# Kernel optimization log

Hardware: AMD Instinct MI355X
Metric: run time of the kernel (lower is better)

## Reference

```python
import jax, jax.numpy as jnp
import numpy as np


def setup_inputs() -> dict:
    key = jax.random.key(0)
    k1, k2, k3, k4, k5 = jax.random.split(key, 5)
    B, S, E, H, D = 8, 1024, 1024, 8, 128  # batch, seq, embed, heads, hidden/head
    stdv = 1.0 / np.sqrt(D)
    return {
        "k": jax.random.normal(k1, (B, S, E), jnp.float32),
        "q": jax.random.normal(k2, (B, S, E), jnp.float32),
        "flag": 0,  # False: project q through w_qx
        "w_kx": jax.random.uniform(k3, (H, E, D), jnp.float32, -stdv, stdv),
        "w_qx": jax.random.uniform(k4, (H, E, D), jnp.float32, -stdv, stdv),
        "proj_w": jax.random.normal(k5, (E, H * D), jnp.float32) * 0.02,  # out_dim = embed_dim
        "proj_b": jnp.zeros((E,), jnp.float32),
    }


def reference(k, q, flag, w_kx, w_qx, proj_w, proj_b):
    H, E, D = w_kx.shape
    B, Sk, _ = k.shape
    Sq = q.shape[1]
    # per-head tanh projections: [H, B, S, D]
    kx = jnp.tanh(jnp.einsum("bse,hed->hbsd", k, w_kx))
    if flag:
        qx = jnp.broadcast_to(q[None], (H,) + q.shape)  # q already in hidden space
    else:
        qx = jnp.tanh(jnp.einsum("bse,hed->hbsd", q, w_qx))
    # scaled dot product scores [H, B, Sq, Sk]
    score = jnp.einsum("hbqd,hbkd->hbqk", qx, kx) / jnp.sqrt(jnp.float32(D))
    attn = jax.nn.softmax(score, axis=-1)
    out = jnp.einsum("hbqk,hbkd->hbqd", attn, kx)  # [H, B, Sq, D]
    # concat heads: [B, Sq, H*D], then output projection (dropout p=0 is identity)
    out = jnp.transpose(out, (1, 2, 0, 3)).reshape(B, Sq, H * D)
    return out @ proj_w.T + proj_b
```

## Files before the change

### kernel.cpp

```cpp
#include <hip/hip_runtime.h>

typedef unsigned short u16;
typedef unsigned int u32;
typedef __bf16 bf16x8 __attribute__((ext_vector_type(8)));
typedef float f32x4 __attribute__((ext_vector_type(4)));

#define MFMA16(a, b, c) __builtin_amdgcn_mfma_f32_16x16x32_bf16(a, b, c, 0, 0, 0)
#define EXP2(x) __builtin_amdgcn_exp2f(x)

typedef const void __attribute__((address_space(1)))* gas1_t;
typedef void __attribute__((address_space(3)))* las3_t;

__device__ __forceinline__ void gload16(const void* g, void* l) {
  __builtin_amdgcn_global_load_lds((gas1_t)g, (las3_t)l, 16, 0, 0);
}

__device__ __forceinline__ u16 f2bf(float f) {
  union { float f; u32 u; } v; v.f = f;
  u32 r = v.u + 0x7FFFu + ((v.u >> 16) & 1u);
  return (u16)(r >> 16);
}

__device__ __forceinline__ float fast_tanh(float x) {
  float xc = fminf(fmaxf(x, -20.f), 20.f);
  float t = EXP2(xc * 2.885390081777927f);
  return (t - 1.0f) * __builtin_amdgcn_rcpf(t + 1.0f);
}

__global__ __launch_bounds__(256) void cvt_kernel(const float* __restrict__ in,
                                                  u16* __restrict__ out, int n8) {
  int i = blockIdx.x * blockDim.x + threadIdx.x;
  int stride = gridDim.x * blockDim.x;
  for (; i < n8; i += stride) {
    const float4* p = (const float4*)(in + (size_t)i * 8);
    float4 a = p[0], b = p[1];
    u16 t[8];
    t[0] = f2bf(a.x); t[1] = f2bf(a.y); t[2] = f2bf(a.z); t[3] = f2bf(a.w);
    t[4] = f2bf(b.x); t[5] = f2bf(b.y); t[6] = f2bf(b.z); t[7] = f2bf(b.w);
    *(uint4*)(out + (size_t)i * 8) = *(uint4*)t;
  }
}

__global__ __launch_bounds__(256) void wtrans_kernel(const float* __restrict__ w,
                                                     u16* __restrict__ wT) {
  __shared__ float t[64][65];
  int h = blockIdx.z;
  int e0 = blockIdx.x * 64, d0 = blockIdx.y * 64;
  const float* src = w + (size_t)h * 1024 * 128;
  u16* dst = wT + (size_t)h * 128 * 1024;
  int tid = threadIdx.x;
  {
    int row = tid >> 2, c0 = (tid & 3) * 16;
#pragma unroll
    for (int i = 0; i < 4; ++i) {
      float4 v = *(const float4*)(src + (size_t)(e0 + row) * 128 + d0 + c0 + i * 4);
      t[row][c0 + i * 4 + 0] = v.x;
      t[row][c0 + i * 4 + 1] = v.y;
      t[row][c0 + i * 4 + 2] = v.z;
      t[row][c0 + i * 4 + 3] = v.w;
    }
  }
  __syncthreads();
  {
    int dl = tid >> 2, c0 = (tid & 3) * 16;
    u16 tmp[16];
#pragma unroll
    for (int i = 0; i < 16; ++i) tmp[i] = f2bf(t[c0 + i][dl]);
    u16* o = dst + (size_t)(d0 + dl) * 1024 + e0 + c0;
    *(uint4*)o = *(uint4*)tmp;
    *(uint4*)(o + 8) = *(uint4*)(tmp + 8);
  }
}

__device__ __forceinline__ void gemm_core128(const u16* Abase, const u16* Bbase,
                                             int K, u16* Alds, u16* Blds,
                                             f32x4 (&acc)[4][4]) {
  const int tid = threadIdx.x, lane = tid & 63, wid = tid >> 6;
  const int wr = wid >> 1, wc = wid & 1;
  const int nkt = K >> 6;
  for (int kt = 0; kt < nkt; ++kt) {
#pragma unroll
    for (int i = 0; i < 4; ++i) {
      int cIdx = (wid * 4 + i) * 64 + lane;
      int row = cIdx >> 3, slot = cIdx & 7;
      int src = slot ^ (row & 7);
      gload16((const char*)Abase + ((size_t)row * K + kt * 64 + src * 8) * 2,
              (char*)Alds + (wid * 4 + i) * 1024);
      gload16((const char*)Bbase + ((size_t)row * K + kt * 64 + src * 8) * 2,
              (char*)Blds + (wid * 4 + i) * 1024);
    }
    __syncthreads();
#pragma unroll
    for (int kc = 0; kc < 2; ++kc) {
      bf16x8 af[4], bb[4];
#pragma unroll
      for (int f = 0; f < 4; ++f) {
        int arow = wr * 64 + f * 16 + (lane & 15);
        int ch = kc * 4 + (lane >> 4);
        af[f] = *(const bf16x8*)(Alds + arow * 64 + ((ch ^ (arow & 7)) << 3));
        int brow = wc * 64 + f * 16 + (lane & 15);
        bb[f] = *(const bf16x8*)(Blds + brow * 64 + ((ch ^ (brow & 7)) << 3));
      }
#pragma unroll
      for (int mf = 0; mf < 4; ++mf)
#pragma unroll
        for (int nf = 0; nf < 4; ++nf)
          acc[mf][nf] = MFMA16(af[mf], bb[nf], acc[mf][nf]);
    }
    __syncthreads();
  }
}

__global__ __launch_bounds__(256) void gemm_tanh_kernel(
    const u16* __restrict__ Ak, const u16* __restrict__ Aq,
    const u16* __restrict__ wTk, const u16* __restrict__ wTq,
    u16* __restrict__ kxo, u16* __restrict__ qxo) {
  __shared__ alignas(16) u16 Alds[128 * 64];
  __shared__ alignas(16) u16 Blds[128 * 64];
  const u16* A; const u16* W; u16* C;
  if (blockIdx.z == 0) { A = Ak; W = wTk; C = kxo; }
  else { A = Aq; W = wTq; C = qxo; }
  int h = blockIdx.y;
  int mBase = blockIdx.x * 128;
  f32x4 acc[4][4];
#pragma unroll
  for (int i = 0; i < 4; ++i)
#pragma unroll
    for (int j = 0; j < 4; ++j) acc[i][j] = (f32x4){0.f, 0.f, 0.f, 0.f};
  gemm_core128(A + (size_t)mBase * 1024, W + (size_t)h * 128 * 1024, 1024,
               Alds, Blds, acc);
  const int lane = threadIdx.x & 63, wid = threadIdx.x >> 6;
  const int wr = wid >> 1, wc = wid & 1;
  u16* Ch = C + (size_t)h * 8192 * 128;
#pragma unroll
  for (int mf = 0; mf < 4; ++mf)
#pragma unroll
    for (int nf = 0; nf < 4; ++nf)
#pragma unroll
      for (int j = 0; j < 4; ++j) {
        int m = mBase + wr * 64 + mf * 16 + ((lane >> 4) << 2) + j;
        int d = wc * 64 + nf * 16 + (lane & 15);
        Ch[(size_t)m * 128 + d] = f2bf(fast_tanh(acc[mf][nf][j]));
      }
}

__global__ __launch_bounds__(256) void transpose_kernel(const u16* __restrict__ kx,
                                                        u16* __restrict__ kxT) {
  __shared__ u16 t[64][72];
  int hb = blockIdx.z;
  const u16* src = kx + (size_t)hb * 1024 * 128;
  u16* dst = kxT + (size_t)hb * 128 * 1024;
  int s0 = blockIdx.x * 64, d0 = blockIdx.y * 64;
  int tid = threadIdx.x;
#pragma unroll
  for (int r = 0; r < 2; ++r) {
    int row = r * 32 + (tid >> 3), c8 = (tid & 7) * 8;
    uint4 v = *(const uint4*)(src + (size_t)(s0 + row) * 128 + d0 + c8);
    *(uint4*)&t[row][c8] = v;
  }
  __syncthreads();
#pragma unroll
  for (int r = 0; r < 2; ++r) {
    int dl = r * 32 + (tid >> 3), s8 = (tid & 7) * 8;
    u16 tmp[8];
#pragma unroll
    for (int i = 0; i < 8; ++i) tmp[i] = t[s8 + i][dl];
    *(uint4*)(dst + (size_t)(d0 + dl) * 1024 + s0 + s8) = *(uint4*)tmp;
  }
}

__global__ __launch_bounds__(256, 2) void attn_kernel(const u16* __restrict__ qx,
                                                      const u16* __restrict__ kx,
                                                      const u16* __restrict__ kxT,
                                                      u16* __restrict__ X) {
  __shared__ alignas(16) u16 Klds[2][64 * 128];
  __shared__ alignas(16) u16 Vlds[2][128 * 64];
  __shared__ alignas(16) u16 Plds[4][32 * 64];
  const int tid = threadIdx.x, lane = tid & 63, wid = tid >> 6;
  const int hb = blockIdx.x, qt = blockIdx.y, h = hb >> 3, b = hb & 7;
  const u16* qxh = qx + ((size_t)h * 8192 + (size_t)b * 1024) * 128;
  const u16* kxh = kx + ((size_t)h * 8192 + (size_t)b * 1024) * 128;
  const u16* kxTh = kxT + (size_t)hb * 128 * 1024;
  const int q0 = qt * 128 + wid * 32;
  const float SC = 0.08838834764831845f * 1.44269504088896340f;

#define STAGE(buf, kt_)                                                        \
  do {                                                                         \
    _Pragma("unroll") for (int i_ = 0; i_ < 4; ++i_) {                         \
      int cIdx = (wid * 4 + i_) * 64 + lane;                                   \
      {                                                                        \
        int row = cIdx >> 4, slot = cIdx & 15;                                 \
        int src = slot ^ (row & 7);                                            \
        gload16((const char*)kxh + (size_t)((kt_) * 64 + row) * 256 + src * 16,\
                (char*)&Klds[buf][0] + (wid * 4 + i_) * 1024);                 \
      }                                                                        \
      {                                                                        \
        int row = cIdx >> 3, slot = cIdx & 7;                                  \
        int src = slot ^ (row & 7);                                            \
        gload16((const char*)kxTh + (size_t)row * 2048 + (kt_) * 128 + src * 16,\
                (char*)&Vlds[buf][0] + (wid * 4 + i_) * 1024);                 \
      }                                                                        \
    }                                                                          \
  } while (0)

  bf16x8 qa[2][4];
#pragma unroll
  for (int mf = 0; mf < 2; ++mf)
#pragma unroll
    for (int kc = 0; kc < 4; ++kc)
      qa[mf][kc] = *(const bf16x8*)(qxh + (size_t)(q0 + mf * 16 + (lane & 15)) * 128
                                    + kc * 32 + (lane >> 4) * 8);

  f32x4 os[2][8];
#pragma unroll
  for (int i = 0; i < 2; ++i)
#pragma unroll
    for (int j = 0; j < 8; ++j) os[i][j] = (f32x4){0.f, 0.f, 0.f, 0.f};
  float lsum[8];
#pragma unroll
  for (int i = 0; i < 8; ++i) lsum[i] = 0.f;

  u16* Pw = &Plds[wid][0];

  STAGE(0, 0);

  for (int kt = 0; kt < 16; ++kt) {
    const int cur = kt & 1;
    if (kt < 15) {
      STAGE(cur ^ 1, kt + 1);
      asm volatile("s_waitcnt vmcnt(8)" ::: "memory");
    } else {
      asm volatile("s_waitcnt vmcnt(0)" ::: "memory");
    }
    __builtin_amdgcn_s_barrier();

    const u16* Kc = &Klds[cur][0];
    const u16* Vc = &Vlds[cur][0];

    f32x4 sa[2][4];
#pragma unroll
    for (int i = 0; i < 2; ++i)
#pragma unroll
      for (int j = 0; j < 4; ++j) sa[i][j] = (f32x4){0.f, 0.f, 0.f, 0.f};
#pragma unroll
    for (int kc = 0; kc < 4; ++kc) {
      bf16x8 kb[4];
#pragma unroll
      for (int nf = 0; nf < 4; ++nf) {
        int row = nf * 16 + (lane & 15);
        int ch = kc * 4 + (lane >> 4);
        kb[nf] = *(const bf16x8*)(Kc + row * 128 + ((ch ^ (row & 7)) << 3));
      }
#pragma unroll
      for (int mf = 0; mf < 2; ++mf)
#pragma unroll
        for (int nf = 0; nf < 4; ++nf)
          sa[mf][nf] = MFMA16(qa[mf][kc], kb[nf], sa[mf][nf]);
    }

#pragma unroll
    for (int mf = 0; mf < 2; ++mf)
#pragma unroll
      for (int j = 0; j < 4; ++j) {
        int ri = mf * 4 + j;
        float p0 = EXP2(sa[mf][0][j] * SC);
        float p1 = EXP2(sa[mf][1][j] * SC);
        float p2 = EXP2(sa[mf][2][j] * SC);
        float p3 = EXP2(sa[mf][3][j] * SC);
        lsum[ri] += (p0 + p1) + (p2 + p3);
        int prow = mf * 16 + (lane >> 4) * 4 + j;
        float pv[4] = {p0, p1, p2, p3};
#pragma unroll
        for (int nf = 0; nf < 4; ++nf) {
          int col = nf * 16 + (lane & 15);
          int byte = prow * 128 + (((col >> 3) ^ (prow & 7)) << 4) + (col & 7) * 2;
          *(u16*)((char*)Pw + byte) = f2bf(pv[nf]);
        }
      }

#pragma unroll
    for (int kc2 = 0; kc2 < 2; ++kc2) {
      bf16x8 pa[2], vb[8];
#pragma unroll
      for (int mf = 0; mf < 2; ++mf) {
        int row = mf * 16 + (lane & 15);
        int ch = kc2 * 4 + (lane >> 4);
        pa[mf] = *(const bf16x8*)(Pw + row * 64 + ((ch ^ (row & 7)) << 3));
      }
#pragma unroll
      for (int nd = 0; nd < 8; ++nd) {
        int row = nd * 16 + (lane & 15);
        int ch = kc2 * 4 + (lane >> 4);
        vb[nd] = *(const bf16x8*)(Vc + row * 64 + ((ch ^ (row & 7)) << 3));
      }
#pragma unroll
      for (int mf = 0; mf < 2; ++mf)
#pragma unroll
        for (int nd = 0; nd < 8; ++nd)
          os[mf][nd] = MFMA16(pa[mf], vb[nd], os[mf][nd]);
    }
    __builtin_amdgcn_s_barrier();
  }
#undef STAGE

#pragma unroll
  for (int ri = 0; ri < 8; ++ri) {
    float s = lsum[ri];
    s += __shfl_xor(s, 1);
    s += __shfl_xor(s, 2);
    s += __shfl_xor(s, 4);
    s += __shfl_xor(s, 8);
    lsum[ri] = s;
  }

#pragma unroll
  for (int mf = 0; mf < 2; ++mf)
#pragma unroll
    for (int j = 0; j < 4; ++j) {
      float inv = 1.f / lsum[mf * 4 + j];
      int m = b * 1024 + q0 + mf * 16 + (lane >> 4) * 4 + j;
#pragma unroll
      for (int nd = 0; nd < 8; ++nd) {
        int col = h * 128 + nd * 16 + (lane & 15);
        X[(size_t)m * 1024 + col] = f2bf(os[mf][nd][j] * inv);
      }
    }
}

__global__ __launch_bounds__(256) void gemm_bias_kernel(
    const u16* __restrict__ X, const u16* __restrict__ pw,
    const float* __restrict__ pb, float* __restrict__ out) {
  __shared__ alignas(16) u16 Alds[128 * 64];
  __shared__ alignas(16) u16 Blds[128 * 64];
  int mBase = blockIdx.x * 128;
  int nBase = blockIdx.y * 128;
  f32x4 acc[4][4];
#pragma unroll
  for (int i = 0; i < 4; ++i)
#pragma unroll
    for (int j = 0; j < 4; ++j) acc[i][j] = (f32x4){0.f, 0.f, 0.f, 0.f};
  gemm_core128(X + (size_t)mBase * 1024, pw + (size_t)nBase * 1024, 1024,
               Alds, Blds, acc);
  const int lane = threadIdx.x & 63, wid = threadIdx.x >> 6;
  const int wr = wid >> 1, wc = wid & 1;
#pragma unroll
  for (int nf = 0; nf < 4; ++nf) {
    int e = nBase + wc * 64 + nf * 16 + (lane & 15);
    float bv = pb[e];
#pragma unroll
    for (int mf = 0; mf < 4; ++mf)
#pragma unroll
      for (int j = 0; j < 4; ++j) {
        int m = mBase + wr * 64 + mf * 16 + ((lane >> 4) << 2) + j;
        out[(size_t)m * 1024 + e] = acc[mf][nf][j] + bv;
      }
  }
}

extern "C" void kernel_launch(void* const* d_in, const int* in_sizes, int n_in,
                              void* d_out, int out_size, void* d_ws, size_t ws_size,
                              hipStream_t stream) {
  const float* k = (const float*)d_in[0];
  const float* q = (const float*)d_in[1];
  const float* wk = (const float*)d_in[3];
  const float* wq = (const float*)d_in[4];
  const float* pw = (const float*)d_in[5];
  const float* pb = (const float*)d_in[6];
  float* out = (float*)d_out;
  char* ws = (char*)d_ws;

  u16* kbf = (u16*)(ws);
  u16* qbf = (u16*)(ws + (16ull << 20));
  u16* wTk = (u16*)(ws + (32ull << 20));
  u16* wTq = (u16*)(ws + (34ull << 20));
  u16* pwb = (u16*)(ws + (36ull << 20));
  u16* kx  = (u16*)(ws + (38ull << 20));
  u16* qx  = (u16*)(ws + (54ull << 20));
  u16* kxT = (u16*)(ws + (70ull << 20));
  u16* X   = kbf;

  cvt_kernel<<<2048, 256, 0, stream>>>(k, kbf, 1048576);
  cvt_kernel<<<2048, 256, 0, stream>>>(q, qbf, 1048576);
  cvt_kernel<<<512, 256, 0, stream>>>(pw, pwb, 131072);
  wtrans_kernel<<<dim3(16, 2, 8), 256, 0, stream>>>(wk, wTk);
  wtrans_kernel<<<dim3(16, 2, 8), 256, 0, stream>>>(wq, wTq);
  gemm_tanh_kernel<<<dim3(64, 8, 2), 256, 0, stream>>>(kbf, qbf, wTk, wTq, kx, qx);
  transpose_kernel<<<dim3(16, 2, 64), 256, 0, stream>>>(kx, kxT);
  attn_kernel<<<dim3(64, 8), 256, 0, stream>>>(qx, kx, kxT, X);
  gemm_bias_kernel<<<dim3(64, 8), 256, 0, stream>>>(X, pwb, pb, out);
}
```

Baseline: 151.2 us.

## Double-buffer LDS tiles in GEMM core to overlap global loads with MFMA

Replaces the single-buffered GEMM main loop with a two-stage ping-pong LDS pipeline shared by the tanh projection GEMM and the output projection GEMM. The next K tile is issued with global_load_lds while the MFMAs run on the current buffer, using explicit vmcnt waits and raw barriers, so load latency is hidden behind compute instead of stalling each iteration. This doubles LDS use per block to 64 KB, which may lower occupancy, and the hand-placed waitcnt/barrier ordering has to stay exactly right to avoid races.

```diff
diff --git a/kernel.cpp b/kernel.cpp
--- a/kernel.cpp
+++ b/kernel.cpp
@@ -72,51 +72,74 @@
   }
 }
 
-__device__ __forceinline__ void gemm_core128(const u16* Abase, const u16* Bbase,
-                                             int K, u16* Alds, u16* Blds,
-                                             f32x4 (&acc)[4][4]) {
+__device__ __forceinline__ void gemm_core128_db(const u16* Abase, const u16* Bbase,
+                                                int K,
+                                                u16* A0, u16* B0, u16* A1, u16* B1,
+                                                f32x4 (&acc)[4][4]) {
   const int tid = threadIdx.x, lane = tid & 63, wid = tid >> 6;
   const int wr = wid >> 1, wc = wid & 1;
   const int nkt = K >> 6;
-  for (int kt = 0; kt < nkt; ++kt) {
-#pragma unroll
-    for (int i = 0; i < 4; ++i) {
-      int cIdx = (wid * 4 + i) * 64 + lane;
-      int row = cIdx >> 3, slot = cIdx & 7;
-      int src = slot ^ (row & 7);
-      gload16((const char*)Abase + ((size_t)row * K + kt * 64 + src * 8) * 2,
-              (char*)Alds + (wid * 4 + i) * 1024);
-      gload16((const char*)Bbase + ((size_t)row * K + kt * 64 + src * 8) * 2,
-              (char*)Blds + (wid * 4 + i) * 1024);
-    }
-    __syncthreads();
-#pragma unroll
-    for (int kc = 0; kc < 2; ++kc) {
-      bf16x8 af[4], bb[4];
-#pragma unroll
-      for (int f = 0; f < 4; ++f) {
-        int arow = wr * 64 + f * 16 + (lane & 15);
-        int ch = kc * 4 + (lane >> 4);
-        af[f] = *(const bf16x8*)(Alds + arow * 64 + ((ch ^ (arow & 7)) << 3));
-        int brow = wc * 64 + f * 16 + (lane & 15);
-        bb[f] = *(const bf16x8*)(Blds + brow * 64 + ((ch ^ (brow & 7)) << 3));
-      }
-#pragma unroll
-      for (int mf = 0; mf < 4; ++mf)
-#pragma unroll
-        for (int nf = 0; nf < 4; ++nf)
-          acc[mf][nf] = MFMA16(af[mf], bb[nf], acc[mf][nf]);
-    }
-    __syncthreads();
-  }
+
+#define GSTAGE(Al, Bl, kt_)                                                     \
+  do {                                                                          \
+    _Pragma("unroll") for (int i_ = 0; i_ < 4; ++i_) {                          \
+      int cIdx = (wid * 4 + i_) * 64 + lane;                                    \
+      int row = cIdx >> 3, slot = cIdx & 7;                                     \
+      int src = slot ^ (row & 7);                                               \
+      gload16((const char*)Abase + ((size_t)row * K + (kt_) * 64 + src * 8) * 2,\
+              (char*)(Al) + (wid * 4 + i_) * 1024);                             \
+      gload16((const char*)Bbase + ((size_t)row * K + (kt_) * 64 + src * 8) * 2,\
+              (char*)(Bl) + (wid * 4 + i_) * 1024);                             \
+    }                                                                           \
+  } while (0)
+
+#define GCOMPUTE(Al, Bl)                                                        \
+  do {                                                                          \
+    _Pragma("unroll") for (int kc = 0; kc < 2; ++kc) {                          \
+      bf16x8 af[4], bb[4];                                                      \
+      _Pragma("unroll") for (int f = 0; f < 4; ++f) {                           \
+        int arow = wr * 64 + f * 16 + (lane & 15);                              \
+        int ch = kc * 4 + (lane >> 4);                                          \
+        af[f] = *(const bf16x8*)((Al) + arow * 64 + ((ch ^ (arow & 7)) << 3));  \
+        int brow = wc * 64 + f * 16 + (lane & 15);                              \
+        bb[f] = *(const bf16x8*)((Bl) + brow * 64 + ((ch ^ (brow & 7)) << 3));  \
+      }                                                                         \
+      _Pragma("unroll") for (int mf = 0; mf < 4; ++mf)                          \
+        _Pragma("unroll") for (int nf = 0; nf < 4; ++nf)                        \
+          acc[mf][nf] = MFMA16(af[mf], bb[nf], acc[mf][nf]);                    \
+    }                                                                           \
+  } while (0)
+
+  GSTAGE(A0, B0, 0);
+  for (int it = 0; it < nkt / 2 - 1; ++it) {
+    GSTAGE(A1, B1, 2 * it + 1);
+    asm volatile("s_waitcnt vmcnt(8)" ::: "memory");
+    __builtin_amdgcn_s_barrier();
+    GCOMPUTE(A0, B0);
+    __builtin_amdgcn_s_barrier();
+    GSTAGE(A0, B0, 2 * it + 2);
+    asm volatile("s_waitcnt vmcnt(8)" ::: "memory");
+    __builtin_amdgcn_s_barrier();
+    GCOMPUTE(A1, B1);
+    __builtin_amdgcn_s_barrier();
+  }
+  GSTAGE(A1, B1, nkt - 1);
+  asm volatile("s_waitcnt vmcnt(8)" ::: "memory");
+  __builtin_amdgcn_s_barrier();
+  GCOMPUTE(A0, B0);
+  asm volatile("s_waitcnt vmcnt(0)" ::: "memory");
+  __builtin_amdgcn_s_barrier();
+  GCOMPUTE(A1, B1);
+#undef GSTAGE
+#undef GCOMPUTE
 }
 
 __global__ __launch_bounds__(256) void gemm_tanh_kernel(
     const u16* __restrict__ Ak, const u16* __restrict__ Aq,
     const u16* __restrict__ wTk, const u16* __restrict__ wTq,
     u16* __restrict__ kxo, u16* __restrict__ qxo) {
-  __shared__ alignas(16) u16 Alds[128 * 64];
-  __shared__ alignas(16) u16 Blds[128 * 64];
+  __shared__ alignas(16) u16 A0[128 * 64], B0[128 * 64];
+  __shared__ alignas(16) u16 A1[128 * 64], B1[128 * 64];
   const u16* A; const u16* W; u16* C;
   if (blockIdx.z == 0) { A = Ak; W = wTk; C = kxo; }
   else { A = Aq; W = wTq; C = qxo; }
@@ -127,8 +150,8 @@
   for (int i = 0; i < 4; ++i)
 #pragma unroll
     for (int j = 0; j < 4; ++j) acc[i][j] = (f32x4){0.f, 0.f, 0.f, 0.f};
-  gemm_core128(A + (size_t)mBase * 1024, W + (size_t)h * 128 * 1024, 1024,
-               Alds, Blds, acc);
+  gemm_core128_db(A + (size_t)mBase * 1024, W + (size_t)h * 128 * 1024, 1024,
+                  A0, B0, A1, B1, acc);
   const int lane = threadIdx.x & 63, wid = threadIdx.x >> 6;
   const int wr = wid >> 1, wc = wid & 1;
   u16* Ch = C + (size_t)h * 8192 * 128;
@@ -330,8 +353,8 @@
 __global__ __launch_bounds__(256) void gemm_bias_kernel(
     const u16* __restrict__ X, const u16* __restrict__ pw,
     const float* __restrict__ pb, float* __restrict__ out) {
-  __shared__ alignas(16) u16 Alds[128 * 64];
-  __shared__ alignas(16) u16 Blds[128 * 64];
+  __shared__ alignas(16) u16 A0[128 * 64], B0[128 * 64];
+  __shared__ alignas(16) u16 A1[128 * 64], B1[128 * 64];
   int mBase = blockIdx.x * 128;
   int nBase = blockIdx.y * 128;
   f32x4 acc[4][4];
@@ -339,8 +362,8 @@
   for (int i = 0; i < 4; ++i)
 #pragma unroll
     for (int j = 0; j < 4; ++j) acc[i][j] = (f32x4){0.f, 0.f, 0.f, 0.f};
-  gemm_core128(X + (size_t)mBase * 1024, pw + (size_t)nBase * 1024, 1024,
-               Alds, Blds, acc);
+  gemm_core128_db(X + (size_t)mBase * 1024, pw + (size_t)nBase * 1024, 1024,
+                  A0, B0, A1, B1, acc);
   const int lane = threadIdx.x & 63, wid = threadIdx.x >> 6;
   const int wr = wid >> 1, wc = wid & 1;
 #pragma unroll
```

After: 141.3 us. 1.07x faster.
